# Kernel tuning notes

Hardware: AMD Instinct MI355X
Metric: run time of the kernel (lower is better)

## Reference

```python
import jax, jax.numpy as jnp
import numpy as np

B, S, N, F = 4, 8, 1024, 6
H, L, K, D = 64, 3, 16, 3  # hidden, layers, neighbors, num_dims
EPS = 1e-6


def setup_inputs() -> dict:
    key = jax.random.key(0)
    ks = iter(jax.random.split(key, 64))

    def w(shape, fan_in):
        return jax.random.normal(next(ks), shape, jnp.float32) / np.sqrt(fan_in)

    inp = {
        'points': jax.random.normal(next(ks), (B, S, N, F), jnp.float32),
        'w_in': w((F, H), F), 'b_in': jnp.zeros((H,), jnp.float32),
        # stacked per-layer params for the 3 PointTransformerLayers
        'Wq': w((L, H, H), H), 'bq': jnp.zeros((L, H), jnp.float32),
        'Wk': w((L, H, H), H), 'bk': jnp.zeros((L, H), jnp.float32),
        'Wv': w((L, H, H), H), 'bv': jnp.zeros((L, H), jnp.float32),
        'Wpe': w((L, D, H), D), 'bpe': jnp.zeros((L, H), jnp.float32),
        'Wpd': w((L, D, H), D), 'bpd': jnp.zeros((L, H), jnp.float32),
        'Wa': w((L, H, 1), H), 'ba': jnp.zeros((L, 1), jnp.float32),
        'Wo': w((L, H, H), H), 'bo': jnp.zeros((L, H), jnp.float32),
        'ln_s': jnp.ones((L, H), jnp.float32), 'ln_b': jnp.zeros((L, H), jnp.float32),
        # EncoderTransformerLayer params
        'Wek': w((H, H), H), 'bek': jnp.zeros((H,), jnp.float32),
        'Weq': w((H, H), H), 'beq': jnp.zeros((H,), jnp.float32),
        'Wev': w((H, H), H), 'bev': jnp.zeros((H,), jnp.float32),
        'We1': w((H, H), H), 'be1': jnp.zeros((H,), jnp.float32),
        'We2': w((H, H), H), 'be2': jnp.zeros((H,), jnp.float32),
        'ln2_s': jnp.ones((H,), jnp.float32), 'ln2_b': jnp.zeros((H,), jnp.float32),
    }
    return inp


def _layernorm(x, scale, bias):
    mu = jnp.mean(x, axis=-1, keepdims=True)
    var = jnp.var(x, axis=-1, keepdims=True)
    return (x - mu) * jax.lax.rsqrt(var + EPS) * scale + bias


def _point_layer(x, pos, Wq, bq, Wk, bk, Wv, bv, Wpe, bpe, Wpd, bpd, Wa, ba, Wo, bo):
    # x: [B,S,N,H], pos: [B,S,N,3]
    q = x @ Wq + bq
    k = x @ Wk + bk
    v = x @ Wv + bv
    pos_enc = pos @ Wpe + bpe  # [B,S,N,H]
    # pairwise squared distances: diff[i,j] = pos[i] - pos[j]
    pos_diff = pos[..., :, None, :] - pos[..., None, :, :]  # [B,S,N,N,3]
    dist = jnp.sum(pos_diff ** 2, axis=-1)                  # [B,S,N,N]
    _, nidx = jax.lax.top_k(-dist, K)                       # [B,S,N,K]

    def gather(a):  # a: [B,S,N,C] -> [B,S,N,K,C]
        return jnp.take_along_axis(a[:, :, None], nidx[..., None], axis=3)

    k_n = gather(k)
    v_n = gather(v)
    p_n = gather(pos_enc)
    qp = (q + pos_enc)[..., None, :]                        # [B,S,N,1,H]
    pd_enc = (gather(pos) - pos[..., None, :]) @ Wpd + bpd  # [B,S,N,K,H]
    scale = jnp.sqrt(jnp.float32(H))
    attn = qp * (k_n + p_n + pd_enc) / scale                # [B,S,N,K,H]
    attn = (attn @ Wa + ba).squeeze(-1)                     # [B,S,N,K]
    attn = jax.nn.softmax(attn, axis=-1)
    out = jnp.sum(attn[..., None] * v_n, axis=-2)           # [B,S,N,H]
    out = jax.nn.gelu(out @ Wo + bo)
    return x + out


def _encoder_layer(x, Wek, bek, Weq, beq, Wev, bev, We1, be1, We2, be2):
    k = x @ Wek + bek
    q = x @ Weq + beq
    v = x @ Wev + bev
    aw = jnp.einsum('bth,bsh->bts', q, k)
    aw = jax.nn.softmax(aw / jnp.sqrt(jnp.float32(H)), axis=-1)
    out = jnp.einsum('bts,bsh->bth', aw, v)
    out = jax.nn.gelu(out @ We1 + be1) @ We2 + be2
    return x + out


def reference(points, w_in, b_in, Wq, bq, Wk, bk, Wv, bv, Wpe, bpe, Wpd, bpd,
              Wa, ba, Wo, bo, ln_s, ln_b, Wek, bek, Weq, beq, Wev, bev,
              We1, be1, We2, be2, ln2_s, ln2_b):
    pos = points[..., :D]
    x = points @ w_in + b_in
    for i in range(L):
        x = _point_layer(x, pos, Wq[i], bq[i], Wk[i], bk[i], Wv[i], bv[i],
                         Wpe[i], bpe[i], Wpd[i], bpd[i], Wa[i], ba[i], Wo[i], bo[i])
        x = _layernorm(x, ln_s[i], ln_b[i])
    x = jnp.max(x, axis=-2)  # pool over points -> [B,S,H]
    x = _encoder_layer(x, Wek, bek, Weq, beq, Wev, bev, We1, be1, We2, be2)
    x = _layernorm(x, ln2_s, ln2_b)
    x = jnp.max(x, axis=-2)  # pool over seq -> [B,H]
    return x
```

## Files before the change

### kernel.cpp

```cpp
#include <hip/hip_runtime.h>
#include <cfloat>
#include <cmath>
#include <cstdint>

#define NPT   1024
#define NCL   32
#define PTOT  32768
#define HH    64
#define KNN_K 16
#define KNN_BLKS (NCL * 256)

#define RFL(x) __builtin_amdgcn_readfirstlane(x)

__device__ __forceinline__ float wave_sum64(float t) {
#pragma unroll
  for (int o = 32; o > 0; o >>= 1) t += __shfl_xor(t, o, 64);
  return t;
}

template <int NV>
__device__ __forceinline__ float mreduce(const float (&P)[NV], int lane) {
  float buf[NV];
#pragma unroll
  for (int i = 0; i < NV; ++i) buf[i] = P[i];
#pragma unroll
  for (int s = 0; (1 << s) < NV; ++s) {
    bool hi = (lane & (1 << s)) != 0;
#pragma unroll
    for (int m = 0; m < (NV >> (s + 1)); ++m) {
      float a = buf[2 * m], b = buf[2 * m + 1];
      float keep = hi ? b : a;
      float send = hi ? a : b;
      buf[m] = keep + __shfl_xor(send, 1 << s, 64);
    }
  }
  float t = buf[0];
#pragma unroll
  for (int o = NV; o < 64; o <<= 1) t += __shfl_xor(t, o, 64);
  return t;
}

__device__ __forceinline__ float gelu_f(float z) {
  float zc = 0.7978845608028654f * (z + 0.044715f * z * z * z);
  float t = __expf(2.0f * zc);
  float th = 1.0f - 2.0f / (t + 1.0f);
  return 0.5f * z * (1.0f + th);
}

__global__ __launch_bounds__(256) void k_front(
    const float* __restrict__ pts, const float* __restrict__ w_in,
    const float* __restrict__ b_in, float* __restrict__ x,
    float* __restrict__ pos4, int* __restrict__ nidx) {
  if (blockIdx.x >= KNN_BLKS) {
    int b2 = blockIdx.x - KNN_BLKS;
    int vb = (b2 & 7) * 1024 + (b2 >> 3);
    int p = vb * 4 + (threadIdx.x >> 6);
    int h = threadIdx.x & 63;
    const float* pp = pts + p * 6;
    float acc = b_in[h];
#pragma unroll
    for (int f = 0; f < 6; ++f) acc += pp[f] * w_in[f * HH + h];
    x[p * HH + h] = acc;
    if (h < 4) pos4[p * 4 + h] = (h < 3) ? pp[h] : 0.0f;
    return;
  }

  __shared__ float sx[NPT], sy[NPT], sz[NPT];
  int cloud = blockIdx.x >> 8;
  int qbase = (blockIdx.x & 255) * 4;
  const float* cp = pts + (size_t)cloud * NPT * 6;
  for (int j = threadIdx.x; j < NPT; j += 256) {
    sx[j] = cp[j * 6 + 0];
    sy[j] = cp[j * 6 + 1];
    sz[j] = cp[j * 6 + 2];
  }
  __syncthreads();

  int wv = threadIdx.x >> 6;
  int lane = threadIdx.x & 63;
  int i = qbase + wv;
  float qx = sx[i], qy = sy[i], qz = sz[i];

  unsigned du[16];
#pragma unroll
  for (int c = 0; c < 16; ++c) {
    int j = c * 64 + lane;
    float dx = qx - sx[j], dy = qy - sy[j], dz = qz - sz[j];
    float d2 = __fadd_rn(__fadd_rn(__fmul_rn(dx, dx), __fmul_rn(dy, dy)),
                         __fmul_rn(dz, dz));
    du[c] = __float_as_uint(d2);
  }

  unsigned t = 0u;
#pragma unroll
  for (int bit = 30; bit >= 15; --bit) {
    unsigned tp = t | (1u << bit);
    int cnt = 0;
#pragma unroll
    for (int c = 0; c < 16; ++c)
      cnt += __popcll(__ballot(du[c] < tp));
    if (cnt <= 15) t = tp;
  }

  int obase = (cloud * NPT + i) * KNN_K;
  unsigned long long below = (1ull << lane) - 1ull;
  int slot = 0;
#pragma unroll
  for (int c = 0; c < 16; ++c) {
    bool lt = du[c] < t;
    unsigned long long m = __ballot(lt);
    if (lt) {
      int off = __popcll(m & below);
      nidx[obase + slot + off] = c * 64 + lane;
    }
    slot += __popcll(m);
  }

  int erem = KNN_K - slot;
  unsigned hi_end = t + (1u << 15);
  unsigned bu[16];
#pragma unroll
  for (int c = 0; c < 16; ++c)
    bu[c] = (du[c] >= t && du[c] < hi_end) ? du[c] : 0xFFFFFFFFu;
  for (int r2 = 0; r2 < erem; ++r2) {
    unsigned bd = bu[0];
    int bc = 0;
#pragma unroll
    for (int c = 1; c < 16; ++c) {
      if (bu[c] < bd) { bd = bu[c]; bc = c; }
    }
    unsigned gd = bd;
#pragma unroll
    for (int o = 32; o > 0; o >>= 1) {
      unsigned g2 = (unsigned)__shfl_xor((int)gd, o, 64);
      gd = (g2 < gd) ? g2 : gd;
    }
    int myidx = bc * 64 + lane;
    int gidx = (bd == gd) ? myidx : 0x7fffffff;
#pragma unroll
    for (int o = 32; o > 0; o >>= 1) {
      int g2 = __shfl_xor(gidx, o, 64);
      gidx = (g2 < gidx) ? g2 : gidx;
    }
    if (lane == 0) nidx[obase + slot + r2] = gidx;
    int sel = (myidx == gidx) ? bc : 99;
#pragma unroll
    for (int c = 0; c < 16; ++c) bu[c] = (c == sel) ? 0xFFFFFFFFu : bu[c];
  }
}

__global__ __launch_bounds__(256) void k_qkv_gemm(
    const float* __restrict__ x, const float* __restrict__ pos4,
    const float* __restrict__ Wq, const float* __restrict__ bq,
    const float* __restrict__ Wk, const float* __restrict__ bk,
    const float* __restrict__ Wv, const float* __restrict__ bv,
    const float* __restrict__ Wpe, const float* __restrict__ bpe,
    const float* __restrict__ Wpd, const float* __restrict__ bpd,
    float* __restrict__ qq, float* __restrict__ kkv) {
  int lane = threadIdx.x & 63;
  int bid = blockIdx.x;
  int vb = (bid & 7) * 256 + (bid >> 3);
  int pb = RFL(vb * 16 + (threadIdx.x >> 6) * 4);
  const float* xw = x + (size_t)pb * HH;
  const float4* posw = reinterpret_cast<const float4*>(pos4) + pb;

  float wpe0 = Wpe[lane], wpe1 = Wpe[HH + lane], wpe2 = Wpe[2 * HH + lane];
  float wpd0 = Wpd[lane], wpd1 = Wpd[HH + lane], wpd2 = Wpd[2 * HH + lane];
  float we0 = wpe0 + wpd0, we1 = wpe1 + wpd1, we2 = wpe2 + wpd2;
  float bqq = bq[lane] + bpe[lane];
  float bkk = bk[lane] + bpe[lane] + bpd[lane];
  float bvv = bv[lane];

  float aq[4], ak[4], av[4];
#pragma unroll
  for (int p = 0; p < 4; ++p) { aq[p] = bqq; ak[p] = bkk; av[p] = bvv; }

#pragma unroll
  for (int c = 0; c < 8; ++c) {
    float wq8[8], wk8[8], wv8[8];
#pragma unroll
    for (int j = 0; j < 8; ++j) {
      int g = c * 8 + j;
      wq8[j] = Wq[g * HH + lane];
      wk8[j] = Wk[g * HH + lane];
      wv8[j] = Wv[g * HH + lane];
    }
#pragma unroll
    for (int p = 0; p < 4; ++p) {
#pragma unroll
      for (int j = 0; j < 8; ++j) {
        float xv = xw[p * HH + c * 8 + j];
        aq[p] = fmaf(xv, wq8[j], aq[p]);
        ak[p] = fmaf(xv, wk8[j], ak[p]);
        av[p] = fmaf(xv, wv8[j], av[p]);
      }
    }
  }

#pragma unroll
  for (int p = 0; p < 4; ++p) {
    float4 pp = posw[p];
    float qv = aq[p] + pp.x * wpe0 + pp.y * wpe1 + pp.z * wpe2;
    float kv = ak[p] + pp.x * we0 + pp.y * we1 + pp.z * we2;
    qq[(size_t)(pb + p) * HH + lane] = qv;
    reinterpret_cast<float2*>(kkv + ((size_t)(pb + p) << 7))[lane] =
        make_float2(kv, av[p]);
  }
}

__global__ __launch_bounds__(256) void k_attn_core(
    float* __restrict__ qq, const float* __restrict__ kkv,
    const int* __restrict__ nidx, const float* __restrict__ pos4,
    const float* __restrict__ Wpd, const float* __restrict__ Wa,
    const float* __restrict__ ba) {
  int lane = threadIdx.x & 63;
  int bid = blockIdx.x;
  int vb = (bid & 7) * 1024 + (bid >> 3);
  int pu = RFL(vb * 4 + (threadIdx.x >> 6));
  int cbase = pu & ~(NPT - 1);

  float4 pp = reinterpret_cast<const float4*>(pos4)[pu];
  float u = qq[(size_t)pu * HH + lane] * Wa[lane] * 0.125f;
  float pdq = pp.x * Wpd[lane] + pp.y * Wpd[HH + lane] + pp.z * Wpd[2 * HH + lane];
  float C0 = wave_sum64(u * pdq) - ba[0];

  const int4* niw = reinterpret_cast<const int4*>(nidx + (size_t)pu * KNN_K);
  int nj[KNN_K];
#pragma unroll
  for (int g = 0; g < 4; ++g) {
    int4 r = niw[g];
    nj[g * 4 + 0] = r.x; nj[g * 4 + 1] = r.y;
    nj[g * 4 + 2] = r.z; nj[g * 4 + 3] = r.w;
  }

  float vj[KNN_K], P[KNN_K];
#pragma unroll
  for (int jj = 0; jj < KNN_K; ++jj) {
    float2 kv = reinterpret_cast<const float2*>(
        kkv + ((size_t)(cbase + nj[jj]) << 7))[lane];
    vj[jj] = kv.y;
    P[jj] = u * kv.x;
  }

  float T = mreduce<16>(P, lane);
  float lg = T - C0;

  float mx = lg;
#pragma unroll
  for (int o = 1; o < 16; o <<= 1) mx = fmaxf(mx, __shfl_xor(mx, o, 64));
  float e = __expf(lg - mx);
  float s = e;
#pragma unroll
  for (int o = 1; o < 16; o <<= 1) s += __shfl_xor(s, o, 64);

  float oacc = 0.f;
  int sb = lane & 48;
#pragma unroll
  for (int jj = 0; jj < KNN_K; ++jj)
    oacc = fmaf(__shfl(e, sb | jj, 64), vj[jj], oacc);

  qq[(size_t)pu * HH + lane] = oacc / s;
}

__global__ __launch_bounds__(256) void k_wo_ln(
    const float* __restrict__ outb, const float* __restrict__ Wo,
    const float* __restrict__ bo, float* __restrict__ x,
    const float* __restrict__ ln_s, const float* __restrict__ ln_b,
    float* __restrict__ partial, int do_pool) {
  __shared__ float red[4][HH];
  int lane = threadIdx.x & 63;
  int wv = threadIdx.x >> 6;
  int bid = blockIdx.x;
  int vb = (bid & 7) * 256 + (bid >> 3);
  int pb = RFL(vb * 16 + wv * 4);
  const float* ow = outb + (size_t)pb * HH;

  float acc[4];
  float b0 = bo[lane];
#pragma unroll
  for (int p = 0; p < 4; ++p) acc[p] = b0;

#pragma unroll
  for (int c = 0; c < 8; ++c) {
    float w8[8];
#pragma unroll
    for (int j = 0; j < 8; ++j) w8[j] = Wo[(c * 8 + j) * HH + lane];
#pragma unroll
    for (int p = 0; p < 4; ++p) {
#pragma unroll
      for (int j = 0; j < 8; ++j) {
        float ov = ow[p * HH + c * 8 + j];
        acc[p] = fmaf(ov, w8[j], acc[p]);
      }
    }
  }

  float sg = ln_s[lane], bg = ln_b[lane];
  float xn[4];
#pragma unroll
  for (int p = 0; p < 4; ++p)
    xn[p] = x[(size_t)(pb + p) * HH + lane] + gelu_f(acc[p]);

  float Ts = mreduce<4>(xn, lane);
  float dd[4], sq[4];
#pragma unroll
  for (int p = 0; p < 4; ++p) {
    float mu = __shfl(Ts, p, 64) * (1.0f / HH);
    dd[p] = xn[p] - mu;
    sq[p] = dd[p] * dd[p];
  }
  float Tv = mreduce<4>(sq, lane);
  float mxp = -FLT_MAX;
#pragma unroll
  for (int p = 0; p < 4; ++p) {
    float var = __shfl(Tv, p, 64) * (1.0f / HH);
    float yv = dd[p] * rsqrtf(var + 1e-6f) * sg + bg;
    x[(size_t)(pb + p) * HH + lane] = yv;
    mxp = fmaxf(mxp, yv);
  }

  if (do_pool) {
    red[wv][lane] = mxp;
    __syncthreads();
    if (wv == 0) {
      float m = fmaxf(fmaxf(red[0][lane], red[1][lane]),
                      fmaxf(red[2][lane], red[3][lane]));
      partial[(size_t)vb * HH + lane] = m;
    }
  }
}

__global__ __launch_bounds__(512) void k_enc(
    const float* __restrict__ partial,
    const float* __restrict__ Wek, const float* __restrict__ bek,
    const float* __restrict__ Weq, const float* __restrict__ beq,
    const float* __restrict__ Wev, const float* __restrict__ bev,
    const float* __restrict__ We1, const float* __restrict__ be1,
    const float* __restrict__ We2, const float* __restrict__ be2,
    const float* __restrict__ ln2_s, const float* __restrict__ ln2_b,
    float* __restrict__ out) {
  __shared__ float xs[8][HH], ks[8][HH], vs[8][HH], x2[8][HH];
  int b = blockIdx.x;
  int t = threadIdx.x >> 6;
  int h = threadIdx.x & 63;
  {
    int ci = b * 8 + t;
    const float* pp = partial + (size_t)ci * 64 * HH + h;
    float mx = pp[0];
#pragma unroll
    for (int c8 = 1; c8 < 64; ++c8) mx = fmaxf(mx, pp[c8 * HH]);
    xs[t][h] = mx;
  }
  __syncthreads();

  float kk = bek[h], qq = beq[h], vv = bev[h];
#pragma unroll 8
  for (int g = 0; g < HH; ++g) {
    float xv = xs[t][g];
    kk += xv * Wek[g * HH + h];
    qq += xv * Weq[g * HH + h];
    vv += xv * Wev[g * HH + h];
  }
  ks[t][h] = kk;
  vs[t][h] = vv;
  __syncthreads();

  float logit[8];
#pragma unroll
  for (int s = 0; s < 8; ++s) {
    float tt = qq * ks[s][h];
    logit[s] = wave_sum64(tt) * 0.125f;
  }
  float m = logit[0];
#pragma unroll
  for (int s = 1; s < 8; ++s) m = fmaxf(m, logit[s]);
  float ssum = 0.f;
#pragma unroll
  for (int s = 0; s < 8; ++s) { logit[s] = expf(logit[s] - m); ssum += logit[s]; }
  float o = 0.f;
#pragma unroll
  for (int s = 0; s < 8; ++s) o += (logit[s] / ssum) * vs[s][h];

  float h1 = be1[h];
#pragma unroll 8
  for (int g = 0; g < HH; ++g) h1 += __shfl(o, g, 64) * We1[g * HH + h];
  h1 = gelu_f(h1);
  float h2 = be2[h];
#pragma unroll 8
  for (int g = 0; g < HH; ++g) h2 += __shfl(h1, g, 64) * We2[g * HH + h];

  float xn = xs[t][h] + h2;
  float mu = wave_sum64(xn) * (1.0f / HH);
  float d = xn - mu;
  float var = wave_sum64(d * d) * (1.0f / HH);
  float yv = d * rsqrtf(var + 1e-6f) * ln2_s[h] + ln2_b[h];
  x2[t][h] = yv;
  __syncthreads();
  if (t == 0) {
    float mm = x2[0][h];
#pragma unroll
    for (int s = 1; s < 8; ++s) mm = fmaxf(mm, x2[s][h]);
    out[b * HH + h] = mm;
  }
}

extern "C" void kernel_launch(void* const* d_in, const int* in_sizes, int n_in,
                              void* d_out, int out_size, void* d_ws, size_t ws_size,
                              hipStream_t stream) {
  const float* points = (const float*)d_in[0];
  const float* w_in   = (const float*)d_in[1];
  const float* b_in   = (const float*)d_in[2];
  const float* Wq     = (const float*)d_in[3];
  const float* bq     = (const float*)d_in[4];
  const float* Wk     = (const float*)d_in[5];
  const float* bk     = (const float*)d_in[6];
  const float* Wv     = (const float*)d_in[7];
  const float* bv     = (const float*)d_in[8];
  const float* Wpe    = (const float*)d_in[9];
  const float* bpe    = (const float*)d_in[10];
  const float* Wpd    = (const float*)d_in[11];
  const float* bpd    = (const float*)d_in[12];
  const float* Wa     = (const float*)d_in[13];
  const float* ba     = (const float*)d_in[14];
  const float* Wo     = (const float*)d_in[15];
  const float* bo     = (const float*)d_in[16];
  const float* ln_s   = (const float*)d_in[17];
  const float* ln_b   = (const float*)d_in[18];
  const float* Wek    = (const float*)d_in[19];
  const float* bek    = (const float*)d_in[20];
  const float* Weq    = (const float*)d_in[21];
  const float* beq    = (const float*)d_in[22];
  const float* Wev    = (const float*)d_in[23];
  const float* bev    = (const float*)d_in[24];
  const float* We1    = (const float*)d_in[25];
  const float* be1    = (const float*)d_in[26];
  const float* We2    = (const float*)d_in[27];
  const float* be2    = (const float*)d_in[28];
  const float* ln2_s  = (const float*)d_in[29];
  const float* ln2_b  = (const float*)d_in[30];

  float* ws      = (float*)d_ws;
  float* pos4    = ws;
  float* xbuf    = pos4 + 4 * PTOT;
  float* qbuf    = xbuf + 64 * PTOT;
  float* kkv     = qbuf + 64 * PTOT;
  float* partial = kkv + 128 * PTOT;
  int*   nidx    = (int*)(partial + 2048 * HH);

  k_front<<<KNN_BLKS + PTOT / 4, 256, 0, stream>>>(points, w_in, b_in,
                                                   xbuf, pos4, nidx);

  for (int l = 0; l < 3; ++l) {
    k_qkv_gemm<<<PTOT / 16, 256, 0, stream>>>(xbuf, pos4,
        Wq + l * HH * HH, bq + l * HH,
        Wk + l * HH * HH, bk + l * HH,
        Wv + l * HH * HH, bv + l * HH,
        Wpe + l * 3 * HH, bpe + l * HH,
        Wpd + l * 3 * HH, bpd + l * HH,
        qbuf, kkv);
    k_attn_core<<<PTOT / 4, 256, 0, stream>>>(qbuf, kkv, nidx, pos4,
        Wpd + l * 3 * HH, Wa + l * HH, ba + l);
    k_wo_ln<<<PTOT / 16, 256, 0, stream>>>(qbuf,
        Wo + l * HH * HH, bo + l * HH, xbuf,
        ln_s + l * HH, ln_b + l * HH, partial, l == 2 ? 1 : 0);
  }

  k_enc<<<4, 512, 0, stream>>>(partial, Wek, bek, Weq, beq, Wev, bev,
                               We1, be1, We2, be2, ln2_s, ln2_b, (float*)d_out);
}
```

Measured before the change: 217.5 us.

## Stage GEMM weights in LDS, double points per wave, pack kNN positions as float4

The QKV and Wo/LayerNorm GEMM kernels now copy their 64x64 weight matrices into shared memory once per block and read them from LDS instead of global/L1. Each wave also handles 8 points instead of 4, which halves the grid and raises weight reuse per load. The encoder's pooling reduction is adjusted to the new partial count. Separately, the kNN kernel stores point coordinates as float4 in shared memory so each neighbour needs one vector read. The QKV kernel's 48KB of LDS plus larger register arrays may reduce occupancy, and there are now fewer blocks.

```diff
diff --git a/kernel.cpp b/kernel.cpp
--- a/kernel.cpp
+++ b/kernel.cpp
@@ -65,27 +65,26 @@
     return;
   }
 
-  __shared__ float sx[NPT], sy[NPT], sz[NPT];
+  __shared__ float4 sp[NPT];
   int cloud = blockIdx.x >> 8;
   int qbase = (blockIdx.x & 255) * 4;
   const float* cp = pts + (size_t)cloud * NPT * 6;
   for (int j = threadIdx.x; j < NPT; j += 256) {
-    sx[j] = cp[j * 6 + 0];
-    sy[j] = cp[j * 6 + 1];
-    sz[j] = cp[j * 6 + 2];
+    const float* q = cp + j * 6;
+    sp[j] = make_float4(q[0], q[1], q[2], 0.0f);
   }
   __syncthreads();
 
   int wv = threadIdx.x >> 6;
   int lane = threadIdx.x & 63;
   int i = qbase + wv;
-  float qx = sx[i], qy = sy[i], qz = sz[i];
+  float4 qp = sp[i];
 
   unsigned du[16];
 #pragma unroll
   for (int c = 0; c < 16; ++c) {
-    int j = c * 64 + lane;
-    float dx = qx - sx[j], dy = qy - sy[j], dz = qz - sz[j];
+    float4 pj = sp[c * 64 + lane];
+    float dx = qp.x - pj.x, dy = qp.y - pj.y, dz = qp.z - pj.z;
     float d2 = __fadd_rn(__fadd_rn(__fmul_rn(dx, dx), __fmul_rn(dy, dy)),
                          __fmul_rn(dz, dz));
     du[c] = __float_as_uint(d2);
@@ -157,12 +156,29 @@
     const float* __restrict__ Wpe, const float* __restrict__ bpe,
     const float* __restrict__ Wpd, const float* __restrict__ bpd,
     float* __restrict__ qq, float* __restrict__ kkv) {
+  __shared__ float w_lds[3][HH][HH];
   int lane = threadIdx.x & 63;
+  int wv = threadIdx.x >> 6;
   int bid = blockIdx.x;
-  int vb = (bid & 7) * 256 + (bid >> 3);
-  int pb = RFL(vb * 16 + (threadIdx.x >> 6) * 4);
+  int vb = (bid & 7) * 128 + (bid >> 3);
+  int pb = RFL(vb * 32 + wv * 8);
   const float* xw = x + (size_t)pb * HH;
   const float4* posw = reinterpret_cast<const float4*>(pos4) + pb;
+
+  {
+    float4* dst = reinterpret_cast<float4*>(&w_lds[0][0][0]);
+    const float4* s0 = reinterpret_cast<const float4*>(Wq);
+    const float4* s1 = reinterpret_cast<const float4*>(Wk);
+    const float4* s2 = reinterpret_cast<const float4*>(Wv);
+#pragma unroll
+    for (int i = 0; i < 4; ++i) {
+      int idx = i * 256 + threadIdx.x;
+      dst[idx] = s0[idx];
+      dst[1024 + idx] = s1[idx];
+      dst[2048 + idx] = s2[idx];
+    }
+  }
+  __syncthreads();
 
   float wpe0 = Wpe[lane], wpe1 = Wpe[HH + lane], wpe2 = Wpe[2 * HH + lane];
   float wpd0 = Wpd[lane], wpd1 = Wpd[HH + lane], wpd2 = Wpd[2 * HH + lane];
@@ -171,9 +187,9 @@
   float bkk = bk[lane] + bpe[lane] + bpd[lane];
   float bvv = bv[lane];
 
-  float aq[4], ak[4], av[4];
-#pragma unroll
-  for (int p = 0; p < 4; ++p) { aq[p] = bqq; ak[p] = bkk; av[p] = bvv; }
+  float aq[8], ak[8], av[8];
+#pragma unroll
+  for (int p = 0; p < 8; ++p) { aq[p] = bqq; ak[p] = bkk; av[p] = bvv; }
 
 #pragma unroll
   for (int c = 0; c < 8; ++c) {
@@ -181,12 +197,12 @@
 #pragma unroll
     for (int j = 0; j < 8; ++j) {
       int g = c * 8 + j;
-      wq8[j] = Wq[g * HH + lane];
-      wk8[j] = Wk[g * HH + lane];
-      wv8[j] = Wv[g * HH + lane];
-    }
-#pragma unroll
-    for (int p = 0; p < 4; ++p) {
+      wq8[j] = w_lds[0][g][lane];
+      wk8[j] = w_lds[1][g][lane];
+      wv8[j] = w_lds[2][g][lane];
+    }
+#pragma unroll
+    for (int p = 0; p < 8; ++p) {
 #pragma unroll
       for (int j = 0; j < 8; ++j) {
         float xv = xw[p * HH + c * 8 + j];
@@ -198,7 +214,7 @@
   }
 
 #pragma unroll
-  for (int p = 0; p < 4; ++p) {
+  for (int p = 0; p < 8; ++p) {
     float4 pp = posw[p];
     float qv = aq[p] + pp.x * wpe0 + pp.y * wpe1 + pp.z * wpe2;
     float kv = ak[p] + pp.x * we0 + pp.y * we1 + pp.z * we2;
@@ -267,26 +283,38 @@
     const float* __restrict__ bo, float* __restrict__ x,
     const float* __restrict__ ln_s, const float* __restrict__ ln_b,
     float* __restrict__ partial, int do_pool) {
+  __shared__ float w_lds[HH][HH];
   __shared__ float red[4][HH];
   int lane = threadIdx.x & 63;
   int wv = threadIdx.x >> 6;
   int bid = blockIdx.x;
-  int vb = (bid & 7) * 256 + (bid >> 3);
-  int pb = RFL(vb * 16 + wv * 4);
+  int vb = (bid & 7) * 128 + (bid >> 3);
+  int pb = RFL(vb * 32 + wv * 8);
   const float* ow = outb + (size_t)pb * HH;
 
-  float acc[4];
+  {
+    float4* dst = reinterpret_cast<float4*>(&w_lds[0][0]);
+    const float4* src = reinterpret_cast<const float4*>(Wo);
+#pragma unroll
+    for (int i = 0; i < 4; ++i) {
+      int idx = i * 256 + threadIdx.x;
+      dst[idx] = src[idx];
+    }
+  }
+  __syncthreads();
+
+  float acc[8];
   float b0 = bo[lane];
 #pragma unroll
-  for (int p = 0; p < 4; ++p) acc[p] = b0;
+  for (int p = 0; p < 8; ++p) acc[p] = b0;
 
 #pragma unroll
   for (int c = 0; c < 8; ++c) {
     float w8[8];
 #pragma unroll
-    for (int j = 0; j < 8; ++j) w8[j] = Wo[(c * 8 + j) * HH + lane];
-#pragma unroll
-    for (int p = 0; p < 4; ++p) {
+    for (int j = 0; j < 8; ++j) w8[j] = w_lds[c * 8 + j][lane];
+#pragma unroll
+    for (int p = 0; p < 8; ++p) {
 #pragma unroll
       for (int j = 0; j < 8; ++j) {
         float ov = ow[p * HH + c * 8 + j];
@@ -296,23 +324,23 @@
   }
 
   float sg = ln_s[lane], bg = ln_b[lane];
-  float xn[4];
-#pragma unroll
-  for (int p = 0; p < 4; ++p)
+  float xn[8];
+#pragma unroll
+  for (int p = 0; p < 8; ++p)
     xn[p] = x[(size_t)(pb + p) * HH + lane] + gelu_f(acc[p]);
 
-  float Ts = mreduce<4>(xn, lane);
-  float dd[4], sq[4];
-#pragma unroll
-  for (int p = 0; p < 4; ++p) {
+  float Ts = mreduce<8>(xn, lane);
+  float dd[8], sq[8];
+#pragma unroll
+  for (int p = 0; p < 8; ++p) {
     float mu = __shfl(Ts, p, 64) * (1.0f / HH);
     dd[p] = xn[p] - mu;
     sq[p] = dd[p] * dd[p];
   }
-  float Tv = mreduce<4>(sq, lane);
+  float Tv = mreduce<8>(sq, lane);
   float mxp = -FLT_MAX;
 #pragma unroll
-  for (int p = 0; p < 4; ++p) {
+  for (int p = 0; p < 8; ++p) {
     float var = __shfl(Tv, p, 64) * (1.0f / HH);
     float yv = dd[p] * rsqrtf(var + 1e-6f) * sg + bg;
     x[(size_t)(pb + p) * HH + lane] = yv;
@@ -345,10 +373,10 @@
   int h = threadIdx.x & 63;
   {
     int ci = b * 8 + t;
-    const float* pp = partial + (size_t)ci * 64 * HH + h;
+    const float* pp = partial + (size_t)ci * 32 * HH + h;
     float mx = pp[0];
 #pragma unroll
-    for (int c8 = 1; c8 < 64; ++c8) mx = fmaxf(mx, pp[c8 * HH]);
+    for (int c8 = 1; c8 < 32; ++c8) mx = fmaxf(mx, pp[c8 * HH]);
     xs[t][h] = mx;
   }
   __syncthreads();
@@ -451,7 +479,7 @@
                                                    xbuf, pos4, nidx);
 
   for (int l = 0; l < 3; ++l) {
-    k_qkv_gemm<<<PTOT / 16, 256, 0, stream>>>(xbuf, pos4,
+    k_qkv_gemm<<<1024, 256, 0, stream>>>(xbuf, pos4,
         Wq + l * HH * HH, bq + l * HH,
         Wk + l * HH * HH, bk + l * HH,
         Wv + l * HH * HH, bv + l * HH,
@@ -460,7 +488,7 @@
         qbuf, kkv);
     k_attn_core<<<PTOT / 4, 256, 0, stream>>>(qbuf, kkv, nidx, pos4,
         Wpd + l * 3 * HH, Wa + l * HH, ba + l);
-    k_wo_ln<<<PTOT / 16, 256, 0, stream>>>(qbuf,
+    k_wo_ln<<<1024, 256, 0, stream>>>(qbuf,
         Wo + l * HH * HH, bo + l * HH, xbuf,
         ln_s + l * HH, ln_b + l * HH, partial, l == 2 ? 1 : 0);
   }
```

Measured after the change: 218.8 us. About the same (+0.6%).
